# Performance work log

Measured on AMD Instinct MI355X. Metric: run time of the kernel, lower is better.

## Reference

```python
import jax, jax.numpy as jnp
import numpy as np

N_NODES = 100000
N_EDGES = 1600000
IN_FEATS = 128
HID = 128      # 2 * n_hidden
OUT = 64       # n_hidden


def setup_inputs() -> dict:
    key = jax.random.key(0)
    ks = jax.random.split(key, 10)
    features = jax.random.normal(ks[0], (N_NODES, IN_FEATS), dtype=jnp.float32)
    src = jax.random.randint(ks[1], (N_EDGES,), 0, N_NODES)
    dst = jax.random.randint(ks[2], (N_EDGES,), 0, N_NODES)
    s0 = 1.0 / np.sqrt(IN_FEATS)
    s1 = 1.0 / np.sqrt(HID)
    W_self0 = jax.random.uniform(ks[3], (IN_FEATS, HID), minval=-s0, maxval=s0, dtype=jnp.float32)
    W_neigh0 = jax.random.uniform(ks[4], (IN_FEATS, HID), minval=-s0, maxval=s0, dtype=jnp.float32)
    b0 = jnp.zeros((HID,), dtype=jnp.float32)
    W_self1 = jax.random.uniform(ks[5], (HID, OUT), minval=-s1, maxval=s1, dtype=jnp.float32)
    W_neigh1 = jax.random.uniform(ks[6], (HID, OUT), minval=-s1, maxval=s1, dtype=jnp.float32)
    b1 = jnp.zeros((OUT,), dtype=jnp.float32)
    return {"features": features, "src": src, "dst": dst,
            "W_self0": W_self0, "W_neigh0": W_neigh0, "b0": b0,
            "W_self1": W_self1, "W_neigh1": W_neigh1, "b1": b1}


def _mean_agg(x, src, dst, n_nodes):
    # gather neighbor feats along edges, sum per destination, divide by in-degree
    summed = jax.ops.segment_sum(x[src], dst, num_segments=n_nodes)  # [N, d]
    deg = jax.ops.segment_sum(jnp.ones((src.shape[0],), x.dtype), dst, num_segments=n_nodes)
    deg = jnp.maximum(deg, 1.0)[:, None]
    return summed / deg


def _sage_layer(x, src, dst, W_self, W_neigh, b, act):
    agg = _mean_agg(x, src, dst, x.shape[0])
    out = x @ W_self + agg @ W_neigh + b
    return jax.nn.relu(out) if act else out


def reference(features, src, dst, W_self0, W_neigh0, b0, W_self1, W_neigh1, b1):
    h = _sage_layer(features, src, dst, W_self0, W_neigh0, b0, act=True)
    h = _sage_layer(h, src, dst, W_self1, W_neigh1, b1, act=False)
    return h
```

## Files before the change

### kernel.cpp

```cpp
#include <hip/hip_runtime.h>

#define N_NODES 100000
#define N_EDGES 1600000
#define CAP 60
#define OVF_CAP 8192
#define GBLK 782
#define NBIN 1563
#define NCB 98
#define CCAP 17408
#define BINCAP2 1280
#define FBLK 12500
#define ZROW 100000

typedef unsigned int uint;
typedef unsigned short ushort;
typedef __attribute__((ext_vector_type(8))) short short8;
typedef __attribute__((ext_vector_type(4))) float f32x4;

__device__ __forceinline__ ushort f2bf(float f) {
  uint x = __float_as_uint(f);
  x += 0x7fffu + ((x >> 16) & 1u);
  return (ushort)(x >> 16);
}
__device__ __forceinline__ float bflo(uint u) {
  return __uint_as_float(u << 16);
}
__device__ __forceinline__ float bfhi(uint u) {
  return __uint_as_float(u & 0xffff0000u);
}
__device__ __forceinline__ f32x4 uplo(uint4 u) {
  return (f32x4){bflo(u.x), bfhi(u.x), bflo(u.y), bfhi(u.y)};
}
__device__ __forceinline__ f32x4 uphi(uint4 u) {
  return (f32x4){bflo(u.z), bfhi(u.z), bflo(u.w), bfhi(u.w)};
}

__global__ __launch_bounds__(256) void k_pb(
    const int* __restrict__ src, const int* __restrict__ dst,
    const float* __restrict__ feat, const float* __restrict__ Ws0,
    const float* __restrict__ Wn0, const float* __restrict__ Ws1,
    const float* __restrict__ Wn1, uint* __restrict__ ccur,
    uint* __restrict__ coarse, int* __restrict__ ovf_cnt,
    int* __restrict__ ovf, uint* __restrict__ fbfu, uint* __restrict__ hwu,
    ushort* __restrict__ wp0, ushort* __restrict__ wp1) {
  __shared__ uint hist[NCB];
  int b = blockIdx.x;
  int tid = threadIdx.x;
  if (b < GBLK) {
    if (tid < NCB) hist[tid] = 0;
    __syncthreads();
    int e0 = b * 2048;
    uint val[8], bn[8], rk[8];
    int vld[8];
#pragma unroll
    for (int it = 0; it < 8; ++it) {
      int e = e0 + it * 256 + tid;
      vld[it] = (e < N_EDGES);
      if (vld[it]) {
        uint s = (uint)src[e];
        uint d = (uint)dst[e];
        bn[it] = d >> 10;
        rk[it] = atomicAdd(&hist[bn[it]], 1u);
        val[it] = s | ((d & 1023u) << 17);
      }
    }
    __syncthreads();
    if (tid < NCB) {
      uint h = hist[tid];
      hist[tid] = h ? atomicAdd(&ccur[tid], h) : 0u;
    }
    __syncthreads();
#pragma unroll
    for (int it = 0; it < 8; ++it) {
      if (!vld[it]) continue;
      uint p = hist[bn[it]] + rk[it];
      if (p < CCAP) {
        coarse[(size_t)bn[it] * CCAP + p] = val[it];
      } else {
        int o = atomicAdd(ovf_cnt, 1);
        if (o < OVF_CAP) {
          ovf[2 * o] = (int)(val[it] & 0x1FFFFu);
          ovf[2 * o + 1] = (int)(bn[it] * 1024 + (val[it] >> 17));
        }
      }
    }
    return;
  }
  if (b < GBLK + FBLK) {
    int i = (b - GBLK) * 256 + tid;
    float4 v = reinterpret_cast<const float4*>(feat)[i];
    uint2 o;
    o.x = (uint)f2bf(v.x) | ((uint)f2bf(v.y) << 16);
    o.y = (uint)f2bf(v.z) | ((uint)f2bf(v.w) << 16);
    reinterpret_cast<uint2*>(fbfu)[i] = o;
    return;
  }
  int wb = b - GBLK - FBLK;
  if (wb >= 192) {
    if (tid < 64) fbfu[ZROW * 64 + tid] = 0;
    else if (tid < 96) hwu[ZROW * 32 + (tid - 64)] = 0;
    return;
  }
  int idx = wb * 256 + tid;
  if (idx < 32768) {
    int k = idx >> 7, n = idx & 127;
    float v = (k < 128) ? Ws0[k * 128 + n] : Wn0[(k - 128) * 128 + n];
    int s = k >> 5, q = (k >> 3) & 3, j = k & 7;
    int t = n >> 4, c = n & 15;
    wp0[(((s * 8 + t) * 64) + (q * 16 + c)) * 8 + j] = f2bf(v);
  } else {
    int i2 = idx - 32768;
    int k = i2 >> 7, n = i2 & 127;
    float v = (n < 64) ? Wn1[k * 64 + n] : Ws1[k * 64 + (n - 64)];
    int s = k >> 5, q = (k >> 3) & 3, j = k & 7;
    int t = n >> 4, c = n & 15;
    wp1[(((s * 8 + t) * 64) + (q * 16 + c)) * 8 + j] = f2bf(v);
  }
}

__global__ __launch_bounds__(256) void k_fb(
    const uint* __restrict__ coarse, const uint* __restrict__ ccur,
    uint* __restrict__ gcursor, int* __restrict__ ovf_cnt,
    int* __restrict__ ovf, uint* __restrict__ binbuf) {
  __shared__ uint hist[16];
  int blk = blockIdx.x;
  int tid = threadIdx.x;
  int cb = blk >> 4, q = blk & 15;
  if (tid < 16) hist[tid] = 0;
  __syncthreads();
  int ne = min((int)ccur[cb], CCAP);
  int lo = (q * ne) >> 4, hi = ((q + 1) * ne) >> 4;
  uint val[5], rk[5];
  int bnv[5], vld[5];
#pragma unroll
  for (int it = 0; it < 5; ++it) {
    int i = lo + it * 256 + tid;
    vld[it] = (i < hi);
    if (vld[it]) {
      uint v = coarse[(size_t)cb * CCAP + i];
      uint d10 = v >> 17;
      int f = (int)(d10 >> 6);
      rk[it] = atomicAdd(&hist[f], 1u);
      bnv[it] = f;
      val[it] = (v & 0x1FFFFu) | ((d10 & 63u) << 17);
    }
  }
  __syncthreads();
  if (tid < 16) {
    uint h = hist[tid];
    hist[tid] = h ? atomicAdd(&gcursor[cb * 16 + tid], h) : 0u;
  }
  __syncthreads();
#pragma unroll
  for (int it = 0; it < 5; ++it) {
    if (!vld[it]) continue;
    uint p = hist[bnv[it]] + rk[it];
    int fine = cb * 16 + bnv[it];
    if (p < BINCAP2) {
      binbuf[(size_t)fine * BINCAP2 + p] = val[it];
    } else {
      int o = atomicAdd(ovf_cnt, 1);
      if (o < OVF_CAP) {
        ovf[2 * o] = (int)(val[it] & 0x1FFFFu);
        ovf[2 * o + 1] = fine * 64 + (int)(val[it] >> 17);
      }
    }
  }
}

__global__ __launch_bounds__(256) void k_agg0(
    const uint4* __restrict__ fbf4, const uint* __restrict__ binbuf,
    const uint* __restrict__ gcursor, int* __restrict__ ovf_cnt,
    int* __restrict__ ovf, uint4* __restrict__ agg4) {
  __shared__ __attribute__((aligned(16))) int lbkt[64 * CAP];
  __shared__ uint lcnt[64];
  int bb = blockIdx.x;
  int tid = threadIdx.x;
  if (tid < 64) lcnt[tid] = 0;
#pragma unroll
  for (int i = tid; i < 64 * CAP; i += 256) lbkt[i] = ZROW;
  __syncthreads();
  int ne = min((int)gcursor[bb], BINCAP2);
  for (int i = tid; i < ne; i += 256) {
    uint v = binbuf[(size_t)bb * BINCAP2 + i];
    int ldl = (int)(v >> 17);
    uint pos = atomicAdd(&lcnt[ldl], 1u);
    if (pos < CAP) {
      lbkt[ldl * CAP + pos] = (int)(v & 0x1FFFFu);
    } else {
      int o = atomicAdd(ovf_cnt, 1);
      if (o < OVF_CAP) {
        ovf[2 * o] = (int)(v & 0x1FFFFu);
        ovf[2 * o + 1] = (bb * 64 + ldl) | (1 << 30);
      }
    }
  }
  __syncthreads();
  int g = tid >> 4, li = tid & 15;
  const int4* lb4 = reinterpret_cast<const int4*>(lbkt);
  int oc = min(*ovf_cnt, OVF_CAP);
#pragma unroll
  for (int p = 0; p < 4; ++p) {
    int nl = p * 16 + g;
    int n = bb * 64 + nl;
    int c = (int)lcnt[nl];
    int kb = min(c, CAP);
    f32x4 accA = (f32x4){0.f, 0.f, 0.f, 0.f};
    f32x4 accB = (f32x4){0.f, 0.f, 0.f, 0.f};
    for (int j = 0; j < kb; j += 12) {
      int4 ia = lb4[nl * 15 + (j >> 2)];
      int4 ib = lb4[nl * 15 + (j >> 2) + 1];
      int4 ic = lb4[nl * 15 + (j >> 2) + 2];
      uint4 u0 = fbf4[(size_t)ia.x * 16 + li];
      uint4 u1 = fbf4[(size_t)ia.y * 16 + li];
      uint4 u2 = fbf4[(size_t)ia.z * 16 + li];
      uint4 u3 = fbf4[(size_t)ia.w * 16 + li];
      uint4 u4 = fbf4[(size_t)ib.x * 16 + li];
      uint4 u5 = fbf4[(size_t)ib.y * 16 + li];
      uint4 u6 = fbf4[(size_t)ib.z * 16 + li];
      uint4 u7 = fbf4[(size_t)ib.w * 16 + li];
      uint4 u8 = fbf4[(size_t)ic.x * 16 + li];
      uint4 u9 = fbf4[(size_t)ic.y * 16 + li];
      uint4 ua = fbf4[(size_t)ic.z * 16 + li];
      uint4 ub = fbf4[(size_t)ic.w * 16 + li];
      accA += uplo(u0); accB += uphi(u0);
      accA += uplo(u1); accB += uphi(u1);
      accA += uplo(u2); accB += uphi(u2);
      accA += uplo(u3); accB += uphi(u3);
      accA += uplo(u4); accB += uphi(u4);
      accA += uplo(u5); accB += uphi(u5);
      accA += uplo(u6); accB += uphi(u6);
      accA += uplo(u7); accB += uphi(u7);
      accA += uplo(u8); accB += uphi(u8);
      accA += uplo(u9); accB += uphi(u9);
      accA += uplo(ua); accB += uphi(ua);
      accA += uplo(ub); accB += uphi(ub);
    }
    for (int i = 0; i < oc; ++i) {
      int df = ovf[2 * i + 1];
      if ((df & 0x1FFFF) == n) {
        uint4 u = fbf4[(size_t)ovf[2 * i] * 16 + li];
        accA += uplo(u);
        accB += uphi(u);
        c += ((df >> 30) & 1) ^ 1;
      }
    }
    float inv = 1.f / (float)max(c, 1);
    accA *= inv;
    accB *= inv;
    if (n < N_NODES) {
      uint4 o;
      o.x = (uint)f2bf(accA.x) | ((uint)f2bf(accA.y) << 16);
      o.y = (uint)f2bf(accA.z) | ((uint)f2bf(accA.w) << 16);
      o.z = (uint)f2bf(accB.x) | ((uint)f2bf(accB.y) << 16);
      o.w = (uint)f2bf(accB.z) | ((uint)f2bf(accB.w) << 16);
      agg4[(size_t)n * 16 + li] = o;
    }
  }
}

__global__ __launch_bounds__(256) void k_gemm(
    const ushort* __restrict__ fbf, const ushort* __restrict__ aggb,
    const short8* __restrict__ wp0f, const short8* __restrict__ wp1f,
    const float* __restrict__ b0, const float* __restrict__ b1,
    ushort* __restrict__ hw, float* __restrict__ out) {
  __shared__ ushort htile[128 * 128];
  int tid = threadIdx.x;
  int lane = tid & 63, w = tid >> 6;
  int quad = lane >> 4, lm = lane & 15;
  int rl0 = (w >> 1) * 64;
  int mw = blockIdx.x * 128 + rl0;
  int tgb = (w & 1) * 4;

  f32x4 acc[4][4];
#pragma unroll
  for (int rt = 0; rt < 4; ++rt)
#pragma unroll
    for (int ct = 0; ct < 4; ++ct) acc[rt][ct] = (f32x4){0.f, 0.f, 0.f, 0.f};
  short8 az = {0, 0, 0, 0, 0, 0, 0, 0};

#pragma unroll
  for (int s = 0; s < 8; ++s) {
    const ushort* bsrc = (s < 4) ? fbf : aggb;
    int koff = (s & 3) * 32 + quad * 8;
    short8 a[4];
#pragma unroll
    for (int rt = 0; rt < 4; ++rt) {
      int row = mw + rt * 16 + lm;
      a[rt] = (row < N_NODES)
                  ? *reinterpret_cast<const short8*>(bsrc + (size_t)row * 128 + koff)
                  : az;
    }
#pragma unroll
    for (int ct = 0; ct < 4; ++ct) {
      short8 b = wp0f[(s * 8 + tgb + ct) * 64 + lane];
#pragma unroll
      for (int rt = 0; rt < 4; ++rt)
        acc[rt][ct] =
            __builtin_amdgcn_mfma_f32_16x16x32_bf16(a[rt], b, acc[rt][ct], 0, 0, 0);
    }
  }

  {
    float bv[4];
#pragma unroll
    for (int ct = 0; ct < 4; ++ct) bv[ct] = b0[(tgb + ct) * 16 + lm];
#pragma unroll
    for (int rt = 0; rt < 4; ++rt)
#pragma unroll
      for (int ct = 0; ct < 4; ++ct)
#pragma unroll
        for (int i = 0; i < 4; ++i) {
          int r = rl0 + rt * 16 + quad * 4 + i;
          float v = (blockIdx.x * 128 + r < N_NODES)
                        ? fmaxf(acc[rt][ct][i] + bv[ct], 0.f)
                        : 0.f;
          int col = (tgb + ct) * 16 + lm;
          htile[r * 128 + (col ^ ((r & 15) * 8))] = f2bf(v);
        }
  }
  __syncthreads();

#pragma unroll
  for (int rt = 0; rt < 4; ++rt)
#pragma unroll
    for (int ct = 0; ct < 4; ++ct) acc[rt][ct] = (f32x4){0.f, 0.f, 0.f, 0.f};

#pragma unroll
  for (int s = 0; s < 4; ++s) {
    int koff = s * 32 + quad * 8;
    short8 a[4];
#pragma unroll
    for (int rt = 0; rt < 4; ++rt) {
      int r = rl0 + rt * 16 + lm;
      a[rt] = *reinterpret_cast<const short8*>(
          &htile[r * 128 + (koff ^ ((r & 15) * 8))]);
    }
#pragma unroll
    for (int ct = 0; ct < 4; ++ct) {
      short8 b = wp1f[(s * 8 + tgb + ct) * 64 + lane];
#pragma unroll
      for (int rt = 0; rt < 4; ++rt)
        acc[rt][ct] =
            __builtin_amdgcn_mfma_f32_16x16x32_bf16(a[rt], b, acc[rt][ct], 0, 0, 0);
    }
  }

  if ((w & 1) == 0) {
#pragma unroll
    for (int rt = 0; rt < 4; ++rt)
#pragma unroll
      for (int ct = 0; ct < 4; ++ct)
#pragma unroll
        for (int i = 0; i < 4; ++i) {
          int row = mw + rt * 16 + quad * 4 + i;
          if (row < N_NODES)
            hw[(size_t)row * 64 + ct * 16 + lm] = f2bf(acc[rt][ct][i]);
        }
  } else {
    float bv[4];
#pragma unroll
    for (int ct = 0; ct < 4; ++ct) bv[ct] = b1[ct * 16 + lm];
#pragma unroll
    for (int rt = 0; rt < 4; ++rt)
#pragma unroll
      for (int ct = 0; ct < 4; ++ct)
#pragma unroll
        for (int i = 0; i < 4; ++i) {
          int row = mw + rt * 16 + quad * 4 + i;
          if (row < N_NODES)
            out[(size_t)row * 64 + ct * 16 + lm] = acc[rt][ct][i] + bv[ct];
        }
  }
}

__global__ __launch_bounds__(256) void k_agg1(
    const uint4* __restrict__ hw4, const uint* __restrict__ binbuf,
    const uint* __restrict__ gcursor, int* __restrict__ ovf_cnt,
    int* __restrict__ ovf, float* __restrict__ out) {
  __shared__ __attribute__((aligned(16))) int lbkt[64 * CAP];
  __shared__ uint lcnt[64];
  int bb = blockIdx.x;
  int tid = threadIdx.x;
  if (tid < 64) lcnt[tid] = 0;
#pragma unroll
  for (int i = tid; i < 64 * CAP; i += 256) lbkt[i] = ZROW;
  __syncthreads();
  int ne = min((int)gcursor[bb], BINCAP2);
  for (int i = tid; i < ne; i += 256) {
    uint v = binbuf[(size_t)bb * BINCAP2 + i];
    int ldl = (int)(v >> 17);
    uint pos = atomicAdd(&lcnt[ldl], 1u);
    if (pos < CAP) lbkt[ldl * CAP + pos] = (int)(v & 0x1FFFFu);
  }
  __syncthreads();
  int g = tid >> 3, li = tid & 7;
  const int4* lb4 = reinterpret_cast<const int4*>(lbkt);
  int oc = min(*ovf_cnt, OVF_CAP);
#pragma unroll
  for (int p = 0; p < 2; ++p) {
    int nl = p * 32 + g;
    int n = bb * 64 + nl;
    int c = (int)lcnt[nl];
    int kb = min(c, CAP);
    f32x4 accA = (f32x4){0.f, 0.f, 0.f, 0.f};
    f32x4 accB = (f32x4){0.f, 0.f, 0.f, 0.f};
    for (int j = 0; j < kb; j += 12) {
      int4 ia = lb4[nl * 15 + (j >> 2)];
      int4 ib = lb4[nl * 15 + (j >> 2) + 1];
      int4 ic = lb4[nl * 15 + (j >> 2) + 2];
      uint4 u0 = hw4[(size_t)ia.x * 8 + li];
      uint4 u1 = hw4[(size_t)ia.y * 8 + li];
      uint4 u2 = hw4[(size_t)ia.z * 8 + li];
      uint4 u3 = hw4[(size_t)ia.w * 8 + li];
      uint4 u4 = hw4[(size_t)ib.x * 8 + li];
      uint4 u5 = hw4[(size_t)ib.y * 8 + li];
      uint4 u6 = hw4[(size_t)ib.z * 8 + li];
      uint4 u7 = hw4[(size_t)ib.w * 8 + li];
      uint4 u8 = hw4[(size_t)ic.x * 8 + li];
      uint4 u9 = hw4[(size_t)ic.y * 8 + li];
      uint4 ua = hw4[(size_t)ic.z * 8 + li];
      uint4 ub = hw4[(size_t)ic.w * 8 + li];
      accA += uplo(u0); accB += uphi(u0);
      accA += uplo(u1); accB += uphi(u1);
      accA += uplo(u2); accB += uphi(u2);
      accA += uplo(u3); accB += uphi(u3);
      accA += uplo(u4); accB += uphi(u4);
      accA += uplo(u5); accB += uphi(u5);
      accA += uplo(u6); accB += uphi(u6);
      accA += uplo(u7); accB += uphi(u7);
      accA += uplo(u8); accB += uphi(u8);
      accA += uplo(u9); accB += uphi(u9);
      accA += uplo(ua); accB += uphi(ua);
      accA += uplo(ub); accB += uphi(ub);
    }
    for (int i = 0; i < oc; ++i) {
      int df = ovf[2 * i + 1];
      if ((df & 0x1FFFF) == n) {
        uint4 u = hw4[(size_t)ovf[2 * i] * 8 + li];
        accA += uplo(u);
        accB += uphi(u);
        c += ((df >> 30) & 1) ^ 1;
      }
    }
    if (n < N_NODES) {
      float inv = 1.f / (float)max(c, 1);
      float* op = out + (size_t)n * 64 + li * 8;
      float4 c0 = *reinterpret_cast<float4*>(op);
      float4 c1 = *reinterpret_cast<float4*>(op + 4);
      c0.x += accA.x * inv;
      c0.y += accA.y * inv;
      c0.z += accA.z * inv;
      c0.w += accA.w * inv;
      c1.x += accB.x * inv;
      c1.y += accB.y * inv;
      c1.z += accB.z * inv;
      c1.w += accB.w * inv;
      *reinterpret_cast<float4*>(op) = c0;
      *reinterpret_cast<float4*>(op + 4) = c1;
    }
  }
}

extern "C" void kernel_launch(void* const* d_in, const int* in_sizes, int n_in,
                              void* d_out, int out_size, void* d_ws,
                              size_t ws_size, hipStream_t stream) {
  const float* feat = (const float*)d_in[0];
  const int* src = (const int*)d_in[1];
  const int* dst = (const int*)d_in[2];
  const float* Ws0 = (const float*)d_in[3];
  const float* Wn0 = (const float*)d_in[4];
  const float* b0 = (const float*)d_in[5];
  const float* Ws1 = (const float*)d_in[6];
  const float* Wn1 = (const float*)d_in[7];
  const float* b1 = (const float*)d_in[8];
  char* ws = (char*)d_ws;

  ushort* hbuf = (ushort*)(ws);
  uint* coarse = (uint*)(ws);
  int* ovf_cnt = (int*)(ws + 25600000);
  uint* gcursor = (uint*)(ws + 25600064);
  uint* ccur = (uint*)(ws + 25606336);
  int* ovf = (int*)(ws + 25606784);
  uint* binbuf = (uint*)(ws + 25672320);
  ushort* fbf = (ushort*)(ws + 33674880);
  ushort* hw = (ushort*)(ws + 59275136);
  ushort* wp0 = (ushort*)(ws + 72075264);
  ushort* wp1 = (ushort*)(ws + 72140800);
  float* out = (float*)d_out;

  hipMemsetAsync(ws + 25600000, 0, 6784, stream);
  k_pb<<<GBLK + FBLK + 193, 256, 0, stream>>>(
      src, dst, feat, Ws0, Wn0, Ws1, Wn1, ccur, coarse, ovf_cnt, ovf,
      (uint*)fbf, (uint*)hw, wp0, wp1);
  k_fb<<<NCB * 16, 256, 0, stream>>>(coarse, ccur, gcursor, ovf_cnt, ovf,
                                     binbuf);
  k_agg0<<<NBIN, 256, 0, stream>>>((const uint4*)fbf, binbuf, gcursor, ovf_cnt,
                                   ovf, (uint4*)hbuf);
  k_gemm<<<GBLK, 256, 0, stream>>>(fbf, hbuf, (const short8*)wp0,
                                   (const short8*)wp1, b0, b1, hw, out);
  k_agg1<<<NBIN, 256, 0, stream>>>((const uint4*)hw, binbuf, gcursor, ovf_cnt,
                                   ovf, out);
}
```

Before: 272.2 us.

## Use fewer, larger blocks for two-pass edge binning with re-read instead of register ranks

```diff
diff --git a/kernel.cpp b/kernel.cpp
--- a/kernel.cpp
+++ b/kernel.cpp
@@ -9,6 +9,8 @@
 #define NCB 98
 #define CCAP 17408
 #define BINCAP2 1280
+#define BINB 250
+#define EPB 6400
 #define FBLK 12500
 #define ZROW 100000
 
@@ -46,23 +48,13 @@
   __shared__ uint hist[NCB];
   int b = blockIdx.x;
   int tid = threadIdx.x;
-  if (b < GBLK) {
+  if (b < BINB) {
     if (tid < NCB) hist[tid] = 0;
     __syncthreads();
-    int e0 = b * 2048;
-    uint val[8], bn[8], rk[8];
-    int vld[8];
-#pragma unroll
-    for (int it = 0; it < 8; ++it) {
-      int e = e0 + it * 256 + tid;
-      vld[it] = (e < N_EDGES);
-      if (vld[it]) {
-        uint s = (uint)src[e];
-        uint d = (uint)dst[e];
-        bn[it] = d >> 10;
-        rk[it] = atomicAdd(&hist[bn[it]], 1u);
-        val[it] = s | ((d & 1023u) << 17);
-      }
+    int e0 = b * EPB;
+    for (int it = 0; it < EPB / 256; ++it) {
+      uint d = (uint)dst[e0 + it * 256 + tid];
+      atomicAdd(&hist[d >> 10], 1u);
     }
     __syncthreads();
     if (tid < NCB) {
@@ -70,24 +62,27 @@
       hist[tid] = h ? atomicAdd(&ccur[tid], h) : 0u;
     }
     __syncthreads();
-#pragma unroll
-    for (int it = 0; it < 8; ++it) {
-      if (!vld[it]) continue;
-      uint p = hist[bn[it]] + rk[it];
+    for (int it = 0; it < EPB / 256; ++it) {
+      int e = e0 + it * 256 + tid;
+      uint s = (uint)src[e];
+      uint d = (uint)dst[e];
+      uint bn = d >> 10;
+      uint p = atomicAdd(&hist[bn], 1u);
+      uint val = s | ((d & 1023u) << 17);
       if (p < CCAP) {
-        coarse[(size_t)bn[it] * CCAP + p] = val[it];
+        coarse[(size_t)bn * CCAP + p] = val;
       } else {
         int o = atomicAdd(ovf_cnt, 1);
         if (o < OVF_CAP) {
-          ovf[2 * o] = (int)(val[it] & 0x1FFFFu);
-          ovf[2 * o + 1] = (int)(bn[it] * 1024 + (val[it] >> 17));
+          ovf[2 * o] = (int)(val & 0x1FFFFu);
+          ovf[2 * o + 1] = (int)(bn * 1024 + (val >> 17));
         }
       }
     }
     return;
   }
-  if (b < GBLK + FBLK) {
-    int i = (b - GBLK) * 256 + tid;
+  if (b < BINB + FBLK) {
+    int i = (b - BINB) * 256 + tid;
     float4 v = reinterpret_cast<const float4*>(feat)[i];
     uint2 o;
     o.x = (uint)f2bf(v.x) | ((uint)f2bf(v.y) << 16);
@@ -95,7 +90,7 @@
     reinterpret_cast<uint2*>(fbfu)[i] = o;
     return;
   }
-  int wb = b - GBLK - FBLK;
+  int wb = b - BINB - FBLK;
   if (wb >= 192) {
     if (tid < 64) fbfu[ZROW * 64 + tid] = 0;
     else if (tid < 96) hwu[ZROW * 32 + (tid - 64)] = 0;
@@ -118,51 +113,38 @@
   }
 }
 
-__global__ __launch_bounds__(256) void k_fb(
+__global__ __launch_bounds__(1024) void k_fb(
     const uint* __restrict__ coarse, const uint* __restrict__ ccur,
     uint* __restrict__ gcursor, int* __restrict__ ovf_cnt,
     int* __restrict__ ovf, uint* __restrict__ binbuf) {
   __shared__ uint hist[16];
-  int blk = blockIdx.x;
+  int cb = blockIdx.x;
   int tid = threadIdx.x;
-  int cb = blk >> 4, q = blk & 15;
   if (tid < 16) hist[tid] = 0;
   __syncthreads();
   int ne = min((int)ccur[cb], CCAP);
-  int lo = (q * ne) >> 4, hi = ((q + 1) * ne) >> 4;
-  uint val[5], rk[5];
-  int bnv[5], vld[5];
-#pragma unroll
-  for (int it = 0; it < 5; ++it) {
-    int i = lo + it * 256 + tid;
-    vld[it] = (i < hi);
-    if (vld[it]) {
-      uint v = coarse[(size_t)cb * CCAP + i];
-      uint d10 = v >> 17;
-      int f = (int)(d10 >> 6);
-      rk[it] = atomicAdd(&hist[f], 1u);
-      bnv[it] = f;
-      val[it] = (v & 0x1FFFFu) | ((d10 & 63u) << 17);
-    }
-  }
+  for (int i = tid; i < ne; i += 1024)
+    atomicAdd(&hist[(coarse[(size_t)cb * CCAP + i] >> 17) >> 6], 1u);
   __syncthreads();
   if (tid < 16) {
     uint h = hist[tid];
     hist[tid] = h ? atomicAdd(&gcursor[cb * 16 + tid], h) : 0u;
   }
   __syncthreads();
-#pragma unroll
-  for (int it = 0; it < 5; ++it) {
-    if (!vld[it]) continue;
-    uint p = hist[bnv[it]] + rk[it];
-    int fine = cb * 16 + bnv[it];
+  for (int i = tid; i < ne; i += 1024) {
+    uint v = coarse[(size_t)cb * CCAP + i];
+    uint d10 = v >> 17;
+    int f = (int)(d10 >> 6);
+    uint p = atomicAdd(&hist[f], 1u);
+    uint val = (v & 0x1FFFFu) | ((d10 & 63u) << 17);
+    int fine = cb * 16 + f;
     if (p < BINCAP2) {
-      binbuf[(size_t)fine * BINCAP2 + p] = val[it];
+      binbuf[(size_t)fine * BINCAP2 + p] = val;
     } else {
       int o = atomicAdd(ovf_cnt, 1);
       if (o < OVF_CAP) {
-        ovf[2 * o] = (int)(val[it] & 0x1FFFFu);
-        ovf[2 * o + 1] = fine * 64 + (int)(val[it] >> 17);
+        ovf[2 * o] = (int)(val & 0x1FFFFu);
+        ovf[2 * o + 1] = fine * 64 + (int)(val >> 17);
       }
     }
   }
@@ -490,11 +472,10 @@
   float* out = (float*)d_out;
 
   hipMemsetAsync(ws + 25600000, 0, 6784, stream);
-  k_pb<<<GBLK + FBLK + 193, 256, 0, stream>>>(
+  k_pb<<<BINB + FBLK + 193, 256, 0, stream>>>(
       src, dst, feat, Ws0, Wn0, Ws1, Wn1, ccur, coarse, ovf_cnt, ovf,
       (uint*)fbf, (uint*)hw, wp0, wp1);
-  k_fb<<<NCB * 16, 256, 0, stream>>>(coarse, ccur, gcursor, ovf_cnt, ovf,
-                                     binbuf);
+  k_fb<<<NCB, 1024, 0, stream>>>(coarse, ccur, gcursor, ovf_cnt, ovf, binbuf);
   k_agg0<<<NBIN, 256, 0, stream>>>((const uint4*)fbf, binbuf, gcursor, ovf_cnt,
                                    ovf, (uint4*)hbuf);
   k_gemm<<<GBLK, 256, 0, stream>>>(fbf, hbuf, (const short8*)wp0,
```

Measured after the change: 278.0 us. +2.1%, slower.

## Fuse layer-0 mean aggregation into the GEMM kernel via shared-memory tile

Applied to the files above, without the earlier changes.

```diff
diff --git a/kernel.cpp b/kernel.cpp
--- a/kernel.cpp
+++ b/kernel.cpp
@@ -168,208 +168,217 @@
   }
 }
 
-__global__ __launch_bounds__(256) void k_agg0(
-    const uint4* __restrict__ fbf4, const uint* __restrict__ binbuf,
-    const uint* __restrict__ gcursor, int* __restrict__ ovf_cnt,
-    int* __restrict__ ovf, uint4* __restrict__ agg4) {
-  __shared__ __attribute__((aligned(16))) int lbkt[64 * CAP];
-  __shared__ uint lcnt[64];
+__global__ __launch_bounds__(1024, 8) void k_ag(
+    const ushort* __restrict__ fbf, const uint4* __restrict__ fbf4,
+    const uint* __restrict__ binbuf, const uint* __restrict__ gcursor,
+    int* __restrict__ ovf_cnt, int* __restrict__ ovf,
+    const short8* __restrict__ wp0f, const short8* __restrict__ wp1f,
+    const float* __restrict__ b0, const float* __restrict__ b1,
+    ushort* __restrict__ hw, float* __restrict__ out) {
+  __shared__ __attribute__((aligned(16))) ushort aggt[128 * 128];
+  __shared__ __attribute__((aligned(16))) ushort htile[128 * 128];
+  int* lbkt = (int*)htile;
+  uint* lcnt = (uint*)(htile + 128 * 120);
   int bb = blockIdx.x;
   int tid = threadIdx.x;
-  if (tid < 64) lcnt[tid] = 0;
-#pragma unroll
-  for (int i = tid; i < 64 * CAP; i += 256) lbkt[i] = ZROW;
-  __syncthreads();
-  int ne = min((int)gcursor[bb], BINCAP2);
-  for (int i = tid; i < ne; i += 256) {
-    uint v = binbuf[(size_t)bb * BINCAP2 + i];
-    int ldl = (int)(v >> 17);
-    uint pos = atomicAdd(&lcnt[ldl], 1u);
-    if (pos < CAP) {
-      lbkt[ldl * CAP + pos] = (int)(v & 0x1FFFFu);
-    } else {
-      int o = atomicAdd(ovf_cnt, 1);
-      if (o < OVF_CAP) {
-        ovf[2 * o] = (int)(v & 0x1FFFFu);
-        ovf[2 * o + 1] = (bb * 64 + ldl) | (1 << 30);
-      }
-    }
-  }
-  __syncthreads();
-  int g = tid >> 4, li = tid & 15;
-  const int4* lb4 = reinterpret_cast<const int4*>(lbkt);
-  int oc = min(*ovf_cnt, OVF_CAP);
-#pragma unroll
-  for (int p = 0; p < 4; ++p) {
-    int nl = p * 16 + g;
-    int n = bb * 64 + nl;
-    int c = (int)lcnt[nl];
-    int kb = min(c, CAP);
-    f32x4 accA = (f32x4){0.f, 0.f, 0.f, 0.f};
-    f32x4 accB = (f32x4){0.f, 0.f, 0.f, 0.f};
-    for (int j = 0; j < kb; j += 12) {
-      int4 ia = lb4[nl * 15 + (j >> 2)];
-      int4 ib = lb4[nl * 15 + (j >> 2) + 1];
-      int4 ic = lb4[nl * 15 + (j >> 2) + 2];
-      uint4 u0 = fbf4[(size_t)ia.x * 16 + li];
-      uint4 u1 = fbf4[(size_t)ia.y * 16 + li];
-      uint4 u2 = fbf4[(size_t)ia.z * 16 + li];
-      uint4 u3 = fbf4[(size_t)ia.w * 16 + li];
-      uint4 u4 = fbf4[(size_t)ib.x * 16 + li];
-      uint4 u5 = fbf4[(size_t)ib.y * 16 + li];
-      uint4 u6 = fbf4[(size_t)ib.z * 16 + li];
-      uint4 u7 = fbf4[(size_t)ib.w * 16 + li];
-      uint4 u8 = fbf4[(size_t)ic.x * 16 + li];
-      uint4 u9 = fbf4[(size_t)ic.y * 16 + li];
-      uint4 ua = fbf4[(size_t)ic.z * 16 + li];
-      uint4 ub = fbf4[(size_t)ic.w * 16 + li];
-      accA += uplo(u0); accB += uphi(u0);
-      accA += uplo(u1); accB += uphi(u1);
-      accA += uplo(u2); accB += uphi(u2);
-      accA += uplo(u3); accB += uphi(u3);
-      accA += uplo(u4); accB += uphi(u4);
-      accA += uplo(u5); accB += uphi(u5);
-      accA += uplo(u6); accB += uphi(u6);
-      accA += uplo(u7); accB += uphi(u7);
-      accA += uplo(u8); accB += uphi(u8);
-      accA += uplo(u9); accB += uphi(u9);
-      accA += uplo(ua); accB += uphi(ua);
-      accA += uplo(ub); accB += uphi(ub);
-    }
-    for (int i = 0; i < oc; ++i) {
-      int df = ovf[2 * i + 1];
-      if ((df & 0x1FFFF) == n) {
-        uint4 u = fbf4[(size_t)ovf[2 * i] * 16 + li];
-        accA += uplo(u);
-        accB += uphi(u);
-        c += ((df >> 30) & 1) ^ 1;
-      }
-    }
-    float inv = 1.f / (float)max(c, 1);
-    accA *= inv;
-    accB *= inv;
-    if (n < N_NODES) {
+  if (tid < 128) lcnt[tid] = 0;
+  for (int i = tid; i < 128 * CAP; i += 1024) lbkt[i] = ZROW;
+  __syncthreads();
+#pragma unroll
+  for (int half = 0; half < 2; ++half) {
+    int bin = bb * 2 + half;
+    if (bin >= NBIN) break;
+    int ne = min((int)gcursor[bin], BINCAP2);
+    for (int i = tid; i < ne; i += 1024) {
+      uint v = binbuf[(size_t)bin * BINCAP2 + i];
+      int ldl = half * 64 + (int)(v >> 17);
+      uint pos = atomicAdd(&lcnt[ldl], 1u);
+      if (pos < CAP) {
+        lbkt[ldl * CAP + pos] = (int)(v & 0x1FFFFu);
+      } else {
+        int o = atomicAdd(ovf_cnt, 1);
+        if (o < OVF_CAP) {
+          ovf[2 * o] = (int)(v & 0x1FFFFu);
+          ovf[2 * o + 1] = (bb * 128 + ldl) | (1 << 30);
+        }
+      }
+    }
+  }
+  __syncthreads();
+  {
+    int g16 = tid >> 4, li = tid & 15;
+    const int4* lb4 = reinterpret_cast<const int4*>(lbkt);
+    int oc = min(*ovf_cnt, OVF_CAP);
+#pragma unroll
+    for (int p = 0; p < 2; ++p) {
+      int nl = p * 64 + g16;
+      int n = bb * 128 + nl;
+      int c = (int)lcnt[nl];
+      int kb = min(c, CAP);
+      f32x4 accA = (f32x4){0.f, 0.f, 0.f, 0.f};
+      f32x4 accB = (f32x4){0.f, 0.f, 0.f, 0.f};
+      for (int j = 0; j < kb; j += 12) {
+        int4 ia = lb4[nl * 15 + (j >> 2)];
+        int4 ib = lb4[nl * 15 + (j >> 2) + 1];
+        int4 ic = lb4[nl * 15 + (j >> 2) + 2];
+        uint4 u0 = fbf4[(size_t)ia.x * 16 + li];
+        uint4 u1 = fbf4[(size_t)ia.y * 16 + li];
+        uint4 u2 = fbf4[(size_t)ia.z * 16 + li];
+        uint4 u3 = fbf4[(size_t)ia.w * 16 + li];
+        uint4 u4 = fbf4[(size_t)ib.x * 16 + li];
+        uint4 u5 = fbf4[(size_t)ib.y * 16 + li];
+        uint4 u6 = fbf4[(size_t)ib.z * 16 + li];
+        uint4 u7 = fbf4[(size_t)ib.w * 16 + li];
+        uint4 u8 = fbf4[(size_t)ic.x * 16 + li];
+        uint4 u9 = fbf4[(size_t)ic.y * 16 + li];
+        uint4 ua = fbf4[(size_t)ic.z * 16 + li];
+        uint4 ub = fbf4[(size_t)ic.w * 16 + li];
+        accA += uplo(u0); accB += uphi(u0);
+        accA += uplo(u1); accB += uphi(u1);
+        accA += uplo(u2); accB += uphi(u2);
+        accA += uplo(u3); accB += uphi(u3);
+        accA += uplo(u4); accB += uphi(u4);
+        accA += uplo(u5); accB += uphi(u5);
+        accA += uplo(u6); accB += uphi(u6);
+        accA += uplo(u7); accB += uphi(u7);
+        accA += uplo(u8); accB += uphi(u8);
+        accA += uplo(u9); accB += uphi(u9);
+        accA += uplo(ua); accB += uphi(ua);
+        accA += uplo(ub); accB += uphi(ub);
+      }
+      for (int i = 0; i < oc; ++i) {
+        int df = ovf[2 * i + 1];
+        if ((df & 0x1FFFF) == n) {
+          uint4 u = fbf4[(size_t)ovf[2 * i] * 16 + li];
+          accA += uplo(u);
+          accB += uphi(u);
+          c += ((df >> 30) & 1) ^ 1;
+        }
+      }
+      float inv = 1.f / (float)max(c, 1);
+      accA *= inv;
+      accB *= inv;
       uint4 o;
       o.x = (uint)f2bf(accA.x) | ((uint)f2bf(accA.y) << 16);
       o.y = (uint)f2bf(accA.z) | ((uint)f2bf(accA.w) << 16);
       o.z = (uint)f2bf(accB.x) | ((uint)f2bf(accB.y) << 16);
       o.w = (uint)f2bf(accB.z) | ((uint)f2bf(accB.w) << 16);
-      agg4[(size_t)n * 16 + li] = o;
-    }
-  }
-}
-
-__global__ __launch_bounds__(256) void k_gemm(
-    const ushort* __restrict__ fbf, const ushort* __restrict__ aggb,
-    const short8* __restrict__ wp0f, const short8* __restrict__ wp1f,
-    const float* __restrict__ b0, const float* __restrict__ b1,
-    ushort* __restrict__ hw, float* __restrict__ out) {
-  __shared__ ushort htile[128 * 128];
-  int tid = threadIdx.x;
+      *reinterpret_cast<uint4*>(&aggt[nl * 128 + ((li * 8) ^ ((nl & 15) * 8))]) = o;
+    }
+  }
+  __syncthreads();
+
   int lane = tid & 63, w = tid >> 6;
   int quad = lane >> 4, lm = lane & 15;
-  int rl0 = (w >> 1) * 64;
-  int mw = blockIdx.x * 128 + rl0;
-  int tgb = (w & 1) * 4;
-
-  f32x4 acc[4][4];
-#pragma unroll
-  for (int rt = 0; rt < 4; ++rt)
-#pragma unroll
-    for (int ct = 0; ct < 4; ++ct) acc[rt][ct] = (f32x4){0.f, 0.f, 0.f, 0.f};
+  int wr = w >> 2, wc = w & 3;
+  int rl0 = wr * 32;
+  f32x4 acc[2][2];
+#pragma unroll
+  for (int rt = 0; rt < 2; ++rt)
+#pragma unroll
+    for (int ct = 0; ct < 2; ++ct) acc[rt][ct] = (f32x4){0.f, 0.f, 0.f, 0.f};
   short8 az = {0, 0, 0, 0, 0, 0, 0, 0};
 
 #pragma unroll
   for (int s = 0; s < 8; ++s) {
-    const ushort* bsrc = (s < 4) ? fbf : aggb;
     int koff = (s & 3) * 32 + quad * 8;
-    short8 a[4];
-#pragma unroll
-    for (int rt = 0; rt < 4; ++rt) {
-      int row = mw + rt * 16 + lm;
-      a[rt] = (row < N_NODES)
-                  ? *reinterpret_cast<const short8*>(bsrc + (size_t)row * 128 + koff)
-                  : az;
-    }
-#pragma unroll
-    for (int ct = 0; ct < 4; ++ct) {
-      short8 b = wp0f[(s * 8 + tgb + ct) * 64 + lane];
-#pragma unroll
-      for (int rt = 0; rt < 4; ++rt)
+    short8 a[2];
+    if (s < 4) {
+#pragma unroll
+      for (int rt = 0; rt < 2; ++rt) {
+        int row = bb * 128 + rl0 + rt * 16 + lm;
+        a[rt] = (row < N_NODES)
+                    ? *reinterpret_cast<const short8*>(fbf + (size_t)row * 128 + koff)
+                    : az;
+      }
+    } else {
+#pragma unroll
+      for (int rt = 0; rt < 2; ++rt) {
+        int r = rl0 + rt * 16 + lm;
+        a[rt] = *reinterpret_cast<const short8*>(
+            &aggt[r * 128 + (koff ^ ((r & 15) * 8))]);
+      }
+    }
+#pragma unroll
+    for (int ct = 0; ct < 2; ++ct) {
+      short8 b = wp0f[(s * 8 + wc * 2 + ct) * 64 + lane];
+#pragma unroll
+      for (int rt = 0; rt < 2; ++rt)
         acc[rt][ct] =
             __builtin_amdgcn_mfma_f32_16x16x32_bf16(a[rt], b, acc[rt][ct], 0, 0, 0);
     }
   }
 
   {
-    float bv[4];
-#pragma unroll
-    for (int ct = 0; ct < 4; ++ct) bv[ct] = b0[(tgb + ct) * 16 + lm];
-#pragma unroll
-    for (int rt = 0; rt < 4; ++rt)
-#pragma unroll
-      for (int ct = 0; ct < 4; ++ct)
+    float bv[2];
+#pragma unroll
+    for (int ct = 0; ct < 2; ++ct) bv[ct] = b0[(wc * 2 + ct) * 16 + lm];
+#pragma unroll
+    for (int rt = 0; rt < 2; ++rt)
+#pragma unroll
+      for (int ct = 0; ct < 2; ++ct)
 #pragma unroll
         for (int i = 0; i < 4; ++i) {
           int r = rl0 + rt * 16 + quad * 4 + i;
-          float v = (blockIdx.x * 128 + r < N_NODES)
+          float v = (bb * 128 + r < N_NODES)
                         ? fmaxf(acc[rt][ct][i] + bv[ct], 0.f)
                         : 0.f;
-          int col = (tgb + ct) * 16 + lm;
+          int col = (wc * 2 + ct) * 16 + lm;
           htile[r * 128 + (col ^ ((r & 15) * 8))] = f2bf(v);
         }
   }
   __syncthreads();
 
 #pragma unroll
-  for (int rt = 0; rt < 4; ++rt)
-#pragma unroll
-    for (int ct = 0; ct < 4; ++ct) acc[rt][ct] = (f32x4){0.f, 0.f, 0.f, 0.f};
+  for (int rt = 0; rt < 2; ++rt)
+#pragma unroll
+    for (int ct = 0; ct < 2; ++ct) acc[rt][ct] = (f32x4){0.f, 0.f, 0.f, 0.f};
 
 #pragma unroll
   for (int s = 0; s < 4; ++s) {
     int koff = s * 32 + quad * 8;
-    short8 a[4];
-#pragma unroll
-    for (int rt = 0; rt < 4; ++rt) {
+    short8 a[2];
+#pragma unroll
+    for (int rt = 0; rt < 2; ++rt) {
       int r = rl0 + rt * 16 + lm;
       a[rt] = *reinterpret_cast<const short8*>(
           &htile[r * 128 + (koff ^ ((r & 15) * 8))]);
     }
 #pragma unroll
-    for (int ct = 0; ct < 4; ++ct) {
-      short8 b = wp1f[(s * 8 + tgb + ct) * 64 + lane];
-#pragma unroll
-      for (int rt = 0; rt < 4; ++rt)
+    for (int ct = 0; ct < 2; ++ct) {
+      short8 b = wp1f[(s * 8 + wc * 2 + ct) * 64 + lane];
+#pragma unroll
+      for (int rt = 0; rt < 2; ++rt)
         acc[rt][ct] =
             __builtin_amdgcn_mfma_f32_16x16x32_bf16(a[rt], b, acc[rt][ct], 0, 0, 0);
     }
   }
 
-  if ((w & 1) == 0) {
-#pragma unroll
-    for (int rt = 0; rt < 4; ++rt)
-#pragma unroll
-      for (int ct = 0; ct < 4; ++ct)
+  if (wc < 2) {
+#pragma unroll
+    for (int rt = 0; rt < 2; ++rt)
+#pragma unroll
+      for (int ct = 0; ct < 2; ++ct)
 #pragma unroll
         for (int i = 0; i < 4; ++i) {
-          int row = mw + rt * 16 + quad * 4 + i;
+          int row = bb * 128 + rl0 + rt * 16 + quad * 4 + i;
           if (row < N_NODES)
-            hw[(size_t)row * 64 + ct * 16 + lm] = f2bf(acc[rt][ct][i]);
+            hw[(size_t)row * 64 + (wc * 2 + ct) * 16 + lm] = f2bf(acc[rt][ct][i]);
         }
   } else {
-    float bv[4];
-#pragma unroll
-    for (int ct = 0; ct < 4; ++ct) bv[ct] = b1[ct * 16 + lm];
-#pragma unroll
-    for (int rt = 0; rt < 4; ++rt)
-#pragma unroll
-      for (int ct = 0; ct < 4; ++ct)
+    float bv[2];
+#pragma unroll
+    for (int ct = 0; ct < 2; ++ct) bv[ct] = b1[((wc - 2) * 2 + ct) * 16 + lm];
+#pragma unroll
+    for (int rt = 0; rt < 2; ++rt)
+#pragma unroll
+      for (int ct = 0; ct < 2; ++ct)
 #pragma unroll
         for (int i = 0; i < 4; ++i) {
-          int row = mw + rt * 16 + quad * 4 + i;
+          int row = bb * 128 + rl0 + rt * 16 + quad * 4 + i;
           if (row < N_NODES)
-            out[(size_t)row * 64 + ct * 16 + lm] = acc[rt][ct][i] + bv[ct];
+            out[(size_t)row * 64 + ((wc - 2) * 2 + ct) * 16 + lm] =
+                acc[rt][ct][i] + bv[ct];
         }
   }
 }
@@ -476,7 +485,6 @@
   const float* b1 = (const float*)d_in[8];
   char* ws = (char*)d_ws;
 
-  ushort* hbuf = (ushort*)(ws);
   uint* coarse = (uint*)(ws);
   int* ovf_cnt = (int*)(ws + 25600000);
   uint* gcursor = (uint*)(ws + 25600064);
@@ -495,10 +503,9 @@
       (uint*)fbf, (uint*)hw, wp0, wp1);
   k_fb<<<NCB * 16, 256, 0, stream>>>(coarse, ccur, gcursor, ovf_cnt, ovf,
                                      binbuf);
-  k_agg0<<<NBIN, 256, 0, stream>>>((const uint4*)fbf, binbuf, gcursor, ovf_cnt,
-                                   ovf, (uint4*)hbuf);
-  k_gemm<<<GBLK, 256, 0, stream>>>(fbf, hbuf, (const short8*)wp0,
-                                   (const short8*)wp1, b0, b1, hw, out);
+  k_ag<<<GBLK, 1024, 0, stream>>>(fbf, (const uint4*)fbf, binbuf, gcursor,
+                                  ovf_cnt, ovf, (const short8*)wp0,
+                                  (const short8*)wp1, b0, b1, hw, out);
   k_agg1<<<NBIN, 256, 0, stream>>>((const uint4*)hw, binbuf, gcursor, ovf_cnt,
                                    ovf, out);
 }
```

After: 262.3 us. -3.6%, faster.
